# Performance work log

Hardware: AMD Instinct MI355X
Metric: run time of the kernel (lower is better)

Reference implementation:

```python
import jax, jax.numpy as jnp
import numpy as np

REG = 0.1          # entropic regularization, as in the module
N_ITERS = 100      # fixed Sinkhorn iteration count (POT numItermax capped; see notes)


def _sqdist(x, y):
    # ot.dist default: squared Euclidean pairwise distances, [n, m]
    x2 = jnp.sum(x * x, axis=1)[:, None]
    y2 = jnp.sum(y * y, axis=1)[None, :]
    M = x2 + y2 - 2.0 * (x @ y.T)
    return jnp.maximum(M, 0.0)


def setup_inputs() -> dict:
    key = jax.random.key(0)
    kx, ky = jax.random.split(key)
    n, m, d = 4096, 4096, 32
    # uniform in [0, 0.5) keeps exp(-M/reg) representable in fp32
    x = jax.random.uniform(kx, (n, d), dtype=jnp.float32) * 0.5
    y = jax.random.uniform(ky, (m, d), dtype=jnp.float32) * 0.5
    return {"x": x, "y": y}


def reference(x, y):
    n, m = x.shape[0], y.shape[0]
    a = jnp.full((n,), 1.0 / n, dtype=x.dtype)   # uniform source marginal
    b = jnp.full((m,), 1.0 / m, dtype=y.dtype)   # uniform target marginal
    M = _sqdist(x, y)                            # [n, m] cost
    K = jnp.exp(-M / REG)                        # [n, m] Gibbs kernel

    u0 = jnp.full((n,), 1.0 / n, dtype=x.dtype)
    v0 = jnp.full((m,), 1.0 / m, dtype=y.dtype)

    def step(carry, _):
        u, v = carry
        u = a / (K @ v)      # [n]
        v = b / (K.T @ u)    # [m]
        return (u, v), None

    (u, v), _ = jax.lax.scan(step, (u0, v0), None, length=N_ITERS)
    # transport plan gamma = diag(u) K diag(v), as returned by ot.bregman.sinkhorn
    gamma = u[:, None] * K * v[None, :]
    return gamma
```

## Files before the change

kernel.cpp:

```cpp
#include <hip/hip_runtime.h>
#include <hip/hip_fp16.h>


#define NN 4096
#define MM 4096
#define DD 32
#define N_ITERS 100

static constexpr float INV_REG = 10.0f;
static constexpr float A_MARG  = 1.0f / 4096.0f;
static constexpr float B_MARG  = 1.0f / 4096.0f;

typedef _Float16 h2_t __attribute__((ext_vector_type(2)));

static __device__ __forceinline__ float dot2(unsigned a, unsigned b, float acc) {
#if __has_builtin(__builtin_amdgcn_fdot2)
    return __builtin_amdgcn_fdot2(__builtin_bit_cast(h2_t, a),
                                  __builtin_bit_cast(h2_t, b), acc, false);
#else
    float2 fa = __half22float2(*(const __half2*)&a);
    float2 fb = __half22float2(*(const __half2*)&b);
    acc = fmaf(fa.x, fb.x, acc);
    return fmaf(fa.y, fb.y, acc);
#endif
}

static __device__ __forceinline__ unsigned ld_dev_u32(const unsigned* p) {
    return __hip_atomic_load(p, __ATOMIC_RELAXED, __HIP_MEMORY_SCOPE_AGENT);
}
static __device__ __forceinline__ void st_dev_u32(unsigned* p, unsigned v) {
    __hip_atomic_store(p, v, __ATOMIC_RELAXED, __HIP_MEMORY_SCOPE_AGENT);
}

__global__ void compute_K_half(const float* __restrict__ x, const float* __restrict__ y,
                               __half* __restrict__ Kh, __half* __restrict__ KTh,
                               unsigned* __restrict__ mbu, unsigned* __restrict__ mbv) {
    const int tid = threadIdx.x;
    const int j   = blockIdx.x * 256 + tid;
    const int r0  = blockIdx.y * 16;
    const int z   = blockIdx.z;
    const float* __restrict__ p = z ? y : x;
    const float* __restrict__ q = z ? x : y;
    __half* __restrict__ dst    = z ? KTh : Kh;

    if (z == 0 && blockIdx.y == 0) {
        mbu[j] = 0u;
        mbv[j] = 0u;
    }

    float qv[DD];
    const float4* q4 = (const float4*)(q + (size_t)j * DD);
#pragma unroll
    for (int k = 0; k < DD / 4; ++k) {
        float4 t = q4[k];
        qv[4 * k + 0] = t.x; qv[4 * k + 1] = t.y;
        qv[4 * k + 2] = t.z; qv[4 * k + 3] = t.w;
    }

    __shared__ float ps[16 * DD];
    ps[tid]       = p[(size_t)r0 * DD + tid];
    ps[tid + 256] = p[(size_t)r0 * DD + tid + 256];
    __syncthreads();

#pragma unroll 4
    for (int ii = 0; ii < 16; ++ii) {
        float acc = 0.0f;
#pragma unroll
        for (int k = 0; k < DD; ++k) {
            float d = ps[ii * DD + k] - qv[k];
            acc = fmaf(d, d, acc);
        }
        dst[(size_t)(r0 + ii) * MM + j] = __float2half(__expf(-acc * INV_REG));
    }
}

__global__ void __launch_bounds__(1024, 8)
sinkhorn_persist(const __half* __restrict__ Kh, const __half* __restrict__ KTh,
                 float* __restrict__ u32g, float* __restrict__ v32g,
                 unsigned* __restrict__ mbu, unsigned* __restrict__ mbv) {
    __shared__ __align__(16) __half vlds[MM];
    __shared__ float part[16];
    __shared__ unsigned fb_lds[8];
    const int tid  = threadIdx.x;
    const int lane = tid & 63;
    const int w    = tid >> 6;
    const int rib  = w >> 1;
    const int hlf  = w & 1;
    const int bid  = blockIdx.x;
    const int i    = bid * 8 + rib;
    const int g0   = hlf * 256 + lane;
    const uint4* __restrict__ MU = (const uint4*)(Kh  + (size_t)i * MM);
    const uint4* __restrict__ MV = (const uint4*)(KTh + (size_t)i * MM);
    unsigned short* __restrict__ vlh = (unsigned short*)vlds;

    const uint4 ku0 = MU[g0], ku1 = MU[g0 + 64], ku2 = MU[g0 + 128], ku3 = MU[g0 + 192];
    const uint4 kv0 = MV[g0], kv1 = MV[g0 + 64], kv2 = MV[g0 + 128], kv3 = MV[g0 + 192];

    unsigned histv = 0x10000u;

    for (int t = 0; t < N_ITERS; ++t) {
        if (t == 0) {
            if (tid < 512) {
                const unsigned long long dv =
                    (unsigned long long)__half_as_ushort(__float2half(B_MARG)) *
                    0x0001000100010001ULL;
                ((unsigned long long*)vlds)[2 * tid]     = dv;
                ((unsigned long long*)vlds)[2 * tid + 1] = dv;
            }
            __syncthreads();
        } else {
            if (tid < 512) {
                const unsigned want = (unsigned)(2 * t) & 0x7fffu;
                unsigned g[8];
#pragma unroll
                for (int k = 0; k < 8; ++k) g[k] = ld_dev_u32(mbv + (k << 9) + tid);
                for (;;) {
                    unsigned bad = 0u;
#pragma unroll
                    for (int k = 0; k < 8; ++k)
                        if ((g[k] & 0x7fffu) != want) bad |= 1u << k;
                    if (!bad) break;
                    __builtin_amdgcn_s_sleep(1);
#pragma unroll
                    for (int k = 0; k < 8; ++k)
                        if (bad & (1u << k)) g[k] = ld_dev_u32(mbv + (k << 9) + tid);
                }
                unsigned fzb = 0x8000u;
#pragma unroll
                for (int k = 0; k < 8; ++k) {
                    vlh[(k << 9) + tid] = (unsigned short)(g[k] >> 16);
                    fzb &= g[k];
                }
                const bool allf = __all(fzb != 0u);
                if ((tid & 63) == 0) fb_lds[tid >> 6] = allf ? 1u : 0u;
            }
            __syncthreads();
            if ((t & 1) == 0) {
                if ((fb_lds[0] & fb_lds[1] & fb_lds[2] & fb_lds[3] &
                     fb_lds[4] & fb_lds[5] & fb_lds[6] & fb_lds[7]) != 0u)
                    break;
            }
        }

        {
            const uint4* V = (const uint4*)vlds;
            const uint4 a = V[g0], b = V[g0 + 64], c = V[g0 + 128], d = V[g0 + 192];
            float x0 = 0.f, x1 = 0.f, x2 = 0.f, x3 = 0.f;
            x0 = dot2(ku0.x, a.x, x0); x0 = dot2(ku0.y, a.y, x0);
            x0 = dot2(ku0.z, a.z, x0); x0 = dot2(ku0.w, a.w, x0);
            x1 = dot2(ku1.x, b.x, x1); x1 = dot2(ku1.y, b.y, x1);
            x1 = dot2(ku1.z, b.z, x1); x1 = dot2(ku1.w, b.w, x1);
            x2 = dot2(ku2.x, c.x, x2); x2 = dot2(ku2.y, c.y, x2);
            x2 = dot2(ku2.z, c.z, x2); x2 = dot2(ku2.w, c.w, x2);
            x3 = dot2(ku3.x, d.x, x3); x3 = dot2(ku3.y, d.y, x3);
            x3 = dot2(ku3.z, d.z, x3); x3 = dot2(ku3.w, d.w, x3);
            float acc = (x0 + x1) + (x2 + x3);
#pragma unroll
            for (int off = 32; off > 0; off >>= 1) acc += __shfl_down(acc, off, 64);
            if (lane == 0) part[w] = acc;
        }
        __syncthreads();
        if (tid < 8) {
            float r = A_MARG / (part[2 * tid] + part[2 * tid + 1]);
            u32g[bid * 8 + tid] = r;
            const unsigned val = (unsigned)__half_as_ushort(__float2half(r));
            st_dev_u32(mbu + bid * 8 + tid,
                       (val << 16) | ((unsigned)(2 * t + 1) & 0x7fffu));
        }

        if (tid < 512) {
            const unsigned want = (unsigned)(2 * t + 1) & 0x7fffu;
            unsigned g[8];
#pragma unroll
            for (int k = 0; k < 8; ++k) g[k] = ld_dev_u32(mbu + (k << 9) + tid);
            for (;;) {
                unsigned bad = 0u;
#pragma unroll
                for (int k = 0; k < 8; ++k)
                    if ((g[k] & 0x7fffu) != want) bad |= 1u << k;
                if (!bad) break;
                __builtin_amdgcn_s_sleep(1);
#pragma unroll
                for (int k = 0; k < 8; ++k)
                    if (bad & (1u << k)) g[k] = ld_dev_u32(mbu + (k << 9) + tid);
            }
#pragma unroll
            for (int k = 0; k < 8; ++k)
                vlh[(k << 9) + tid] = (unsigned short)(g[k] >> 16);
        }
        __syncthreads();

        {
            const uint4* V = (const uint4*)vlds;
            const uint4 a = V[g0], b = V[g0 + 64], c = V[g0 + 128], d = V[g0 + 192];
            float x0 = 0.f, x1 = 0.f, x2 = 0.f, x3 = 0.f;
            x0 = dot2(kv0.x, a.x, x0); x0 = dot2(kv0.y, a.y, x0);
            x0 = dot2(kv0.z, a.z, x0); x0 = dot2(kv0.w, a.w, x0);
            x1 = dot2(kv1.x, b.x, x1); x1 = dot2(kv1.y, b.y, x1);
            x1 = dot2(kv1.z, b.z, x1); x1 = dot2(kv1.w, b.w, x1);
            x2 = dot2(kv2.x, c.x, x2); x2 = dot2(kv2.y, c.y, x2);
            x2 = dot2(kv2.z, c.z, x2); x2 = dot2(kv2.w, c.w, x2);
            x3 = dot2(kv3.x, d.x, x3); x3 = dot2(kv3.y, d.y, x3);
            x3 = dot2(kv3.z, d.z, x3); x3 = dot2(kv3.w, d.w, x3);
            float acc = (x0 + x1) + (x2 + x3);
#pragma unroll
            for (int off = 32; off > 0; off >>= 1) acc += __shfl_down(acc, off, 64);
            if (lane == 0) part[w] = acc;
        }
        __syncthreads();
        if (tid < 8) {
            float r = B_MARG / (part[2 * tid] + part[2 * tid + 1]);
            v32g[bid * 8 + tid] = r;
            const unsigned val = (unsigned)__half_as_ushort(__float2half(r));
            unsigned ph = (unsigned)(2 * t + 2) & 0x7fffu;
            if (t & 1) {
                if (val == histv) ph |= 0x8000u;
                histv = val;
            }
            st_dev_u32(mbv + bid * 8 + tid, (val << 16) | ph);
        }
    }
}

__global__ void epilogue(const float* __restrict__ x, const float* __restrict__ y,
                         const float* __restrict__ u, const float* __restrict__ v,
                         float* __restrict__ out) {
    const int tid = threadIdx.x;
    const int j   = blockIdx.x * 256 + tid;
    const int r0  = blockIdx.y * 16;

    float yv[DD];
    const float4* y4 = (const float4*)(y + (size_t)j * DD);
#pragma unroll
    for (int k = 0; k < DD / 4; ++k) {
        float4 t = y4[k];
        yv[4 * k + 0] = t.x; yv[4 * k + 1] = t.y;
        yv[4 * k + 2] = t.z; yv[4 * k + 3] = t.w;
    }

    __shared__ float xs[16 * DD];
    __shared__ float u_lds[16];
    xs[tid]       = x[(size_t)r0 * DD + tid];
    xs[tid + 256] = x[(size_t)r0 * DD + tid + 256];
    if (tid < 16) u_lds[tid] = u[r0 + tid];
    __syncthreads();

    const float vj = v[j];
#pragma unroll 4
    for (int ii = 0; ii < 16; ++ii) {
        float acc = 0.0f;
#pragma unroll
        for (int k = 0; k < DD; ++k) {
            float d = xs[ii * DD + k] - yv[k];
            acc = fmaf(d, d, acc);
        }
        out[(size_t)(r0 + ii) * MM + j] = u_lds[ii] * __expf(-acc * INV_REG) * vj;
    }
}

extern "C" void kernel_launch(void* const* d_in, const int* in_sizes, int n_in,
                              void* d_out, int out_size, void* d_ws, size_t ws_size,
                              hipStream_t stream) {
    const float* x = (const float*)d_in[0];
    const float* y = (const float*)d_in[1];
    __half*   Kh   = (__half*)d_ws;
    __half*   KTh  = Kh + (size_t)NN * MM;
    float*    u32  = (float*)(KTh + (size_t)NN * MM);
    float*    v32  = u32 + NN;
    unsigned* mbu  = (unsigned*)(v32 + MM);
    unsigned* mbv  = mbu + NN;
    float*    out  = (float*)d_out;

    compute_K_half<<<dim3(16, 256, 2), 256, 0, stream>>>(x, y, Kh, KTh, mbu, mbv);

    sinkhorn_persist<<<512, 1024, 0, stream>>>(Kh, KTh, u32, v32, mbu, mbv);

    epilogue<<<dim3(MM / 256, NN / 16), 256, 0, stream>>>(x, y, u32, v32, out);
}
```

Measured before the change: 539.4 us.

## Assign one full row per wave and halve persistent grid to 256 blocks

Each wave now owns an entire K and K^T row (8 uint4 chunks per lane held in registers), so the cross-wave partial-sum LDS exchange and its extra __syncthreads are removed. Lane 0 of each wave writes its result directly to the mailbox. Separate LDS buffers for the u and v vectors drop one barrier per half-iteration. The grid shrinks to 256 blocks of 16 rows each, which halves the number of global mailbox pollers, at the cost of higher register pressure (launch bounds lowered to 4) and longer per-wave dot-product chains.

```diff
diff --git a/kernel.cpp b/kernel.cpp
--- a/kernel.cpp
+++ b/kernel.cpp
@@ -74,150 +74,171 @@
     }
 }
 
-__global__ void __launch_bounds__(1024, 8)
+__global__ void __launch_bounds__(1024, 4)
 sinkhorn_persist(const __half* __restrict__ Kh, const __half* __restrict__ KTh,
                  float* __restrict__ u32g, float* __restrict__ v32g,
                  unsigned* __restrict__ mbu, unsigned* __restrict__ mbv) {
-    __shared__ __align__(16) __half vlds[MM];
-    __shared__ float part[16];
-    __shared__ unsigned fb_lds[8];
+    __shared__ __align__(16) __half vbuf0[MM];
+    __shared__ __align__(16) __half vbuf1[MM];
+    __shared__ unsigned fb_lds[16];
     const int tid  = threadIdx.x;
     const int lane = tid & 63;
     const int w    = tid >> 6;
-    const int rib  = w >> 1;
-    const int hlf  = w & 1;
     const int bid  = blockIdx.x;
-    const int i    = bid * 8 + rib;
-    const int g0   = hlf * 256 + lane;
+    const int i    = bid * 16 + w;
     const uint4* __restrict__ MU = (const uint4*)(Kh  + (size_t)i * MM);
     const uint4* __restrict__ MV = (const uint4*)(KTh + (size_t)i * MM);
-    unsigned short* __restrict__ vlh = (unsigned short*)vlds;
-
-    const uint4 ku0 = MU[g0], ku1 = MU[g0 + 64], ku2 = MU[g0 + 128], ku3 = MU[g0 + 192];
-    const uint4 kv0 = MV[g0], kv1 = MV[g0 + 64], kv2 = MV[g0 + 128], kv3 = MV[g0 + 192];
+    unsigned short* __restrict__ vl0 = (unsigned short*)vbuf0;
+    unsigned short* __restrict__ vl1 = (unsigned short*)vbuf1;
+
+    uint4 ku[8], kv[8];
+#pragma unroll
+    for (int c = 0; c < 8; ++c) ku[c] = MU[lane + 64 * c];
+#pragma unroll
+    for (int c = 0; c < 8; ++c) kv[c] = MV[lane + 64 * c];
 
     unsigned histv = 0x10000u;
 
+    {
+        const unsigned long long dv =
+            (unsigned long long)__half_as_ushort(__float2half(B_MARG)) *
+            0x0001000100010001ULL;
+        ((unsigned long long*)vbuf0)[tid] = dv;
+    }
+
     for (int t = 0; t < N_ITERS; ++t) {
-        if (t == 0) {
-            if (tid < 512) {
-                const unsigned long long dv =
-                    (unsigned long long)__half_as_ushort(__float2half(B_MARG)) *
-                    0x0001000100010001ULL;
-                ((unsigned long long*)vlds)[2 * tid]     = dv;
-                ((unsigned long long*)vlds)[2 * tid + 1] = dv;
-            }
-            __syncthreads();
-        } else {
-            if (tid < 512) {
-                const unsigned want = (unsigned)(2 * t) & 0x7fffu;
-                unsigned g[8];
-#pragma unroll
-                for (int k = 0; k < 8; ++k) g[k] = ld_dev_u32(mbv + (k << 9) + tid);
-                for (;;) {
-                    unsigned bad = 0u;
-#pragma unroll
-                    for (int k = 0; k < 8; ++k)
-                        if ((g[k] & 0x7fffu) != want) bad |= 1u << k;
-                    if (!bad) break;
-                    __builtin_amdgcn_s_sleep(1);
-#pragma unroll
-                    for (int k = 0; k < 8; ++k)
-                        if (bad & (1u << k)) g[k] = ld_dev_u32(mbv + (k << 9) + tid);
-                }
-                unsigned fzb = 0x8000u;
-#pragma unroll
-                for (int k = 0; k < 8; ++k) {
-                    vlh[(k << 9) + tid] = (unsigned short)(g[k] >> 16);
-                    fzb &= g[k];
-                }
-                const bool allf = __all(fzb != 0u);
-                if ((tid & 63) == 0) fb_lds[tid >> 6] = allf ? 1u : 0u;
-            }
-            __syncthreads();
-            if ((t & 1) == 0) {
-                if ((fb_lds[0] & fb_lds[1] & fb_lds[2] & fb_lds[3] &
-                     fb_lds[4] & fb_lds[5] & fb_lds[6] & fb_lds[7]) != 0u)
-                    break;
-            }
-        }
-
-        {
-            const uint4* V = (const uint4*)vlds;
-            const uint4 a = V[g0], b = V[g0 + 64], c = V[g0 + 128], d = V[g0 + 192];
-            float x0 = 0.f, x1 = 0.f, x2 = 0.f, x3 = 0.f;
-            x0 = dot2(ku0.x, a.x, x0); x0 = dot2(ku0.y, a.y, x0);
-            x0 = dot2(ku0.z, a.z, x0); x0 = dot2(ku0.w, a.w, x0);
-            x1 = dot2(ku1.x, b.x, x1); x1 = dot2(ku1.y, b.y, x1);
-            x1 = dot2(ku1.z, b.z, x1); x1 = dot2(ku1.w, b.w, x1);
-            x2 = dot2(ku2.x, c.x, x2); x2 = dot2(ku2.y, c.y, x2);
-            x2 = dot2(ku2.z, c.z, x2); x2 = dot2(ku2.w, c.w, x2);
-            x3 = dot2(ku3.x, d.x, x3); x3 = dot2(ku3.y, d.y, x3);
-            x3 = dot2(ku3.z, d.z, x3); x3 = dot2(ku3.w, d.w, x3);
-            float acc = (x0 + x1) + (x2 + x3);
-#pragma unroll
-            for (int off = 32; off > 0; off >>= 1) acc += __shfl_down(acc, off, 64);
-            if (lane == 0) part[w] = acc;
-        }
-        __syncthreads();
-        if (tid < 8) {
-            float r = A_MARG / (part[2 * tid] + part[2 * tid + 1]);
-            u32g[bid * 8 + tid] = r;
-            const unsigned val = (unsigned)__half_as_ushort(__float2half(r));
-            st_dev_u32(mbu + bid * 8 + tid,
-                       (val << 16) | ((unsigned)(2 * t + 1) & 0x7fffu));
-        }
-
-        if (tid < 512) {
-            const unsigned want = (unsigned)(2 * t + 1) & 0x7fffu;
-            unsigned g[8];
-#pragma unroll
-            for (int k = 0; k < 8; ++k) g[k] = ld_dev_u32(mbu + (k << 9) + tid);
+        if (t != 0) {
+            const unsigned want = (unsigned)(2 * t) & 0x7fffu;
+            unsigned g[4];
+#pragma unroll
+            for (int k = 0; k < 4; ++k) g[k] = ld_dev_u32(mbv + (k << 10) + tid);
             for (;;) {
                 unsigned bad = 0u;
 #pragma unroll
-                for (int k = 0; k < 8; ++k)
+                for (int k = 0; k < 4; ++k)
                     if ((g[k] & 0x7fffu) != want) bad |= 1u << k;
                 if (!bad) break;
                 __builtin_amdgcn_s_sleep(1);
 #pragma unroll
-                for (int k = 0; k < 8; ++k)
-                    if (bad & (1u << k)) g[k] = ld_dev_u32(mbu + (k << 9) + tid);
-            }
-#pragma unroll
-            for (int k = 0; k < 8; ++k)
-                vlh[(k << 9) + tid] = (unsigned short)(g[k] >> 16);
+                for (int k = 0; k < 4; ++k)
+                    if (bad & (1u << k)) g[k] = ld_dev_u32(mbv + (k << 10) + tid);
+            }
+            unsigned fzb = 0x8000u;
+#pragma unroll
+            for (int k = 0; k < 4; ++k) {
+                vl0[(k << 10) + tid] = (unsigned short)(g[k] >> 16);
+                fzb &= g[k];
+            }
+            const bool allf = __all(fzb != 0u);
+            if (lane == 0) fb_lds[w] = allf ? 1u : 0u;
         }
         __syncthreads();
+        if (t != 0 && (t & 1) == 0) {
+            unsigned f = 1u;
+#pragma unroll
+            for (int q = 0; q < 16; ++q) f &= fb_lds[q];
+            if (f) break;
+        }
 
         {
-            const uint4* V = (const uint4*)vlds;
-            const uint4 a = V[g0], b = V[g0 + 64], c = V[g0 + 128], d = V[g0 + 192];
+            const uint4* V = (const uint4*)vbuf0;
+            uint4 a0 = V[lane], a1 = V[lane + 64], a2 = V[lane + 128], a3 = V[lane + 192];
+            uint4 a4 = V[lane + 256], a5 = V[lane + 320], a6 = V[lane + 384], a7 = V[lane + 448];
             float x0 = 0.f, x1 = 0.f, x2 = 0.f, x3 = 0.f;
-            x0 = dot2(kv0.x, a.x, x0); x0 = dot2(kv0.y, a.y, x0);
-            x0 = dot2(kv0.z, a.z, x0); x0 = dot2(kv0.w, a.w, x0);
-            x1 = dot2(kv1.x, b.x, x1); x1 = dot2(kv1.y, b.y, x1);
-            x1 = dot2(kv1.z, b.z, x1); x1 = dot2(kv1.w, b.w, x1);
-            x2 = dot2(kv2.x, c.x, x2); x2 = dot2(kv2.y, c.y, x2);
-            x2 = dot2(kv2.z, c.z, x2); x2 = dot2(kv2.w, c.w, x2);
-            x3 = dot2(kv3.x, d.x, x3); x3 = dot2(kv3.y, d.y, x3);
-            x3 = dot2(kv3.z, d.z, x3); x3 = dot2(kv3.w, d.w, x3);
-            float acc = (x0 + x1) + (x2 + x3);
-#pragma unroll
-            for (int off = 32; off > 0; off >>= 1) acc += __shfl_down(acc, off, 64);
-            if (lane == 0) part[w] = acc;
+            float x4 = 0.f, x5 = 0.f, x6 = 0.f, x7 = 0.f;
+            x0 = dot2(ku[0].x, a0.x, x0); x0 = dot2(ku[0].y, a0.y, x0);
+            x0 = dot2(ku[0].z, a0.z, x0); x0 = dot2(ku[0].w, a0.w, x0);
+            x1 = dot2(ku[1].x, a1.x, x1); x1 = dot2(ku[1].y, a1.y, x1);
+            x1 = dot2(ku[1].z, a1.z, x1); x1 = dot2(ku[1].w, a1.w, x1);
+            x2 = dot2(ku[2].x, a2.x, x2); x2 = dot2(ku[2].y, a2.y, x2);
+            x2 = dot2(ku[2].z, a2.z, x2); x2 = dot2(ku[2].w, a2.w, x2);
+            x3 = dot2(ku[3].x, a3.x, x3); x3 = dot2(ku[3].y, a3.y, x3);
+            x3 = dot2(ku[3].z, a3.z, x3); x3 = dot2(ku[3].w, a3.w, x3);
+            x4 = dot2(ku[4].x, a4.x, x4); x4 = dot2(ku[4].y, a4.y, x4);
+            x4 = dot2(ku[4].z, a4.z, x4); x4 = dot2(ku[4].w, a4.w, x4);
+            x5 = dot2(ku[5].x, a5.x, x5); x5 = dot2(ku[5].y, a5.y, x5);
+            x5 = dot2(ku[5].z, a5.z, x5); x5 = dot2(ku[5].w, a5.w, x5);
+            x6 = dot2(ku[6].x, a6.x, x6); x6 = dot2(ku[6].y, a6.y, x6);
+            x6 = dot2(ku[6].z, a6.z, x6); x6 = dot2(ku[6].w, a6.w, x6);
+            x7 = dot2(ku[7].x, a7.x, x7); x7 = dot2(ku[7].y, a7.y, x7);
+            x7 = dot2(ku[7].z, a7.z, x7); x7 = dot2(ku[7].w, a7.w, x7);
+            float s0 = (x0 + x1) + (x2 + x3);
+            float s1 = (x4 + x5) + (x6 + x7);
+#pragma unroll
+            for (int off = 32; off > 0; off >>= 1) {
+                s0 += __shfl_down(s0, off, 64);
+                s1 += __shfl_down(s1, off, 64);
+            }
+            if (lane == 0) {
+                float r = A_MARG / (s0 + s1);
+                u32g[i] = r;
+                const unsigned val = (unsigned)__half_as_ushort(__float2half(r));
+                st_dev_u32(mbu + i, (val << 16) | ((unsigned)(2 * t + 1) & 0x7fffu));
+            }
+        }
+
+        {
+            const unsigned want = (unsigned)(2 * t + 1) & 0x7fffu;
+            unsigned g[4];
+#pragma unroll
+            for (int k = 0; k < 4; ++k) g[k] = ld_dev_u32(mbu + (k << 10) + tid);
+            for (;;) {
+                unsigned bad = 0u;
+#pragma unroll
+                for (int k = 0; k < 4; ++k)
+                    if ((g[k] & 0x7fffu) != want) bad |= 1u << k;
+                if (!bad) break;
+                __builtin_amdgcn_s_sleep(1);
+#pragma unroll
+                for (int k = 0; k < 4; ++k)
+                    if (bad & (1u << k)) g[k] = ld_dev_u32(mbu + (k << 10) + tid);
+            }
+#pragma unroll
+            for (int k = 0; k < 4; ++k)
+                vl1[(k << 10) + tid] = (unsigned short)(g[k] >> 16);
         }
         __syncthreads();
-        if (tid < 8) {
-            float r = B_MARG / (part[2 * tid] + part[2 * tid + 1]);
-            v32g[bid * 8 + tid] = r;
-            const unsigned val = (unsigned)__half_as_ushort(__float2half(r));
-            unsigned ph = (unsigned)(2 * t + 2) & 0x7fffu;
-            if (t & 1) {
-                if (val == histv) ph |= 0x8000u;
-                histv = val;
-            }
-            st_dev_u32(mbv + bid * 8 + tid, (val << 16) | ph);
+
+        {
+            const uint4* V = (const uint4*)vbuf1;
+            uint4 a0 = V[lane], a1 = V[lane + 64], a2 = V[lane + 128], a3 = V[lane + 192];
+            uint4 a4 = V[lane + 256], a5 = V[lane + 320], a6 = V[lane + 384], a7 = V[lane + 448];
+            float x0 = 0.f, x1 = 0.f, x2 = 0.f, x3 = 0.f;
+            float x4 = 0.f, x5 = 0.f, x6 = 0.f, x7 = 0.f;
+            x0 = dot2(kv[0].x, a0.x, x0); x0 = dot2(kv[0].y, a0.y, x0);
+            x0 = dot2(kv[0].z, a0.z, x0); x0 = dot2(kv[0].w, a0.w, x0);
+            x1 = dot2(kv[1].x, a1.x, x1); x1 = dot2(kv[1].y, a1.y, x1);
+            x1 = dot2(kv[1].z, a1.z, x1); x1 = dot2(kv[1].w, a1.w, x1);
+            x2 = dot2(kv[2].x, a2.x, x2); x2 = dot2(kv[2].y, a2.y, x2);
+            x2 = dot2(kv[2].z, a2.z, x2); x2 = dot2(kv[2].w, a2.w, x2);
+            x3 = dot2(kv[3].x, a3.x, x3); x3 = dot2(kv[3].y, a3.y, x3);
+            x3 = dot2(kv[3].z, a3.z, x3); x3 = dot2(kv[3].w, a3.w, x3);
+            x4 = dot2(kv[4].x, a4.x, x4); x4 = dot2(kv[4].y, a4.y, x4);
+            x4 = dot2(kv[4].z, a4.z, x4); x4 = dot2(kv[4].w, a4.w, x4);
+            x5 = dot2(kv[5].x, a5.x, x5); x5 = dot2(kv[5].y, a5.y, x5);
+            x5 = dot2(kv[5].z, a5.z, x5); x5 = dot2(kv[5].w, a5.w, x5);
+            x6 = dot2(kv[6].x, a6.x, x6); x6 = dot2(kv[6].y, a6.y, x6);
+            x6 = dot2(kv[6].z, a6.z, x6); x6 = dot2(kv[6].w, a6.w, x6);
+            x7 = dot2(kv[7].x, a7.x, x7); x7 = dot2(kv[7].y, a7.y, x7);
+            x7 = dot2(kv[7].z, a7.z, x7); x7 = dot2(kv[7].w, a7.w, x7);
+            float s0 = (x0 + x1) + (x2 + x3);
+            float s1 = (x4 + x5) + (x6 + x7);
+#pragma unroll
+            for (int off = 32; off > 0; off >>= 1) {
+                s0 += __shfl_down(s0, off, 64);
+                s1 += __shfl_down(s1, off, 64);
+            }
+            if (lane == 0) {
+                float r = B_MARG / (s0 + s1);
+                v32g[i] = r;
+                const unsigned val = (unsigned)__half_as_ushort(__float2half(r));
+                unsigned ph = (unsigned)(2 * t + 2) & 0x7fffu;
+                if (t & 1) {
+                    if (val == histv) ph |= 0x8000u;
+                    histv = val;
+                }
+                st_dev_u32(mbv + i, (val << 16) | ph);
+            }
         }
     }
 }
@@ -273,7 +294,7 @@
 
     compute_K_half<<<dim3(16, 256, 2), 256, 0, stream>>>(x, y, Kh, KTh, mbu, mbv);
 
-    sinkhorn_persist<<<512, 1024, 0, stream>>>(Kh, KTh, u32, v32, mbu, mbv);
+    sinkhorn_persist<<<256, 1024, 0, stream>>>(Kh, KTh, u32, v32, mbu, mbv);
 
     epilogue<<<dim3(MM / 256, NN / 16), 256, 0, stream>>>(x, y, u32, v32, out);
 }
```

Result: slower. 554.0 us (+2.7%).

## Fuse epilogue into persistent Sinkhorn kernel and widen mailbox polling to 64-bit

Applied to the files above, without the earlier changes.

Folds the transport-plan epilogue into the persistent Sinkhorn kernel. Each block publishes its final fp32 v through a new flag-initialised mailbox and keeps u in registers, which removes a kernel launch and the global u/v round trip. Mailbox polling now uses all 1024 threads with 64-bit relaxed loads instead of 512 threads doing eight 32-bit loads each, which shortens the per-iteration barrier exchange. The trade-off is that the epilogue now runs on only 512 blocks with a wider per-thread loop, which may lower its parallelism.

```diff
diff --git a/kernel.cpp b/kernel.cpp
--- a/kernel.cpp
+++ b/kernel.cpp
@@ -31,10 +31,14 @@
 static __device__ __forceinline__ void st_dev_u32(unsigned* p, unsigned v) {
     __hip_atomic_store(p, v, __ATOMIC_RELAXED, __HIP_MEMORY_SCOPE_AGENT);
 }
+static __device__ __forceinline__ unsigned long long ld_dev_u64(const unsigned long long* p) {
+    return __hip_atomic_load(p, __ATOMIC_RELAXED, __HIP_MEMORY_SCOPE_AGENT);
+}
 
 __global__ void compute_K_half(const float* __restrict__ x, const float* __restrict__ y,
                                __half* __restrict__ Kh, __half* __restrict__ KTh,
-                               unsigned* __restrict__ mbu, unsigned* __restrict__ mbv) {
+                               unsigned* __restrict__ mbu, unsigned* __restrict__ mbv,
+                               unsigned* __restrict__ mbv32) {
     const int tid = threadIdx.x;
     const int j   = blockIdx.x * 256 + tid;
     const int r0  = blockIdx.y * 16;
@@ -44,8 +48,9 @@
     __half* __restrict__ dst    = z ? KTh : Kh;
 
     if (z == 0 && blockIdx.y == 0) {
-        mbu[j] = 0u;
-        mbv[j] = 0u;
+        mbu[j]   = 0u;
+        mbv[j]   = 0u;
+        mbv32[j] = 0xFFFFFFFFu;
     }
 
     float qv[DD];
@@ -75,12 +80,17 @@
 }
 
 __global__ void __launch_bounds__(1024, 8)
-sinkhorn_persist(const __half* __restrict__ Kh, const __half* __restrict__ KTh,
-                 float* __restrict__ u32g, float* __restrict__ v32g,
-                 unsigned* __restrict__ mbu, unsigned* __restrict__ mbv) {
+sinkhorn_all(const float* __restrict__ x, const float* __restrict__ y,
+             const __half* __restrict__ Kh, const __half* __restrict__ KTh,
+             float* __restrict__ out,
+             unsigned* __restrict__ mbu, unsigned* __restrict__ mbv,
+             unsigned* __restrict__ mbv32) {
     __shared__ __align__(16) __half vlds[MM];
+    __shared__ float vfin[MM];
+    __shared__ float xs[8 * DD];
+    __shared__ float ufin[8];
     __shared__ float part[16];
-    __shared__ unsigned fb_lds[8];
+    __shared__ unsigned fb_lds[16];
     const int tid  = threadIdx.x;
     const int lane = tid & 63;
     const int w    = tid >> 6;
@@ -91,55 +101,51 @@
     const int g0   = hlf * 256 + lane;
     const uint4* __restrict__ MU = (const uint4*)(Kh  + (size_t)i * MM);
     const uint4* __restrict__ MV = (const uint4*)(KTh + (size_t)i * MM);
-    unsigned short* __restrict__ vlh = (unsigned short*)vlds;
+    const unsigned long long* __restrict__ mbv64 = (const unsigned long long*)mbv;
+    const unsigned long long* __restrict__ mbu64 = (const unsigned long long*)mbu;
 
     const uint4 ku0 = MU[g0], ku1 = MU[g0 + 64], ku2 = MU[g0 + 128], ku3 = MU[g0 + 192];
     const uint4 kv0 = MV[g0], kv1 = MV[g0 + 64], kv2 = MV[g0 + 128], kv3 = MV[g0 + 192];
 
     unsigned histv = 0x10000u;
+    float u_last = 0.0f, v_last = 0.0f;
+
+    const unsigned long long PHMASK = 0x00007FFF00007FFFull;
+    const unsigned long long FZMASK = 0x0000800000008000ull;
 
     for (int t = 0; t < N_ITERS; ++t) {
         if (t == 0) {
-            if (tid < 512) {
-                const unsigned long long dv =
-                    (unsigned long long)__half_as_ushort(__float2half(B_MARG)) *
-                    0x0001000100010001ULL;
-                ((unsigned long long*)vlds)[2 * tid]     = dv;
-                ((unsigned long long*)vlds)[2 * tid + 1] = dv;
-            }
-            __syncthreads();
+            const unsigned long long dv =
+                (unsigned long long)__half_as_ushort(__float2half(B_MARG)) *
+                0x0001000100010001ULL;
+            ((unsigned long long*)vlds)[tid] = dv;
         } else {
-            if (tid < 512) {
-                const unsigned want = (unsigned)(2 * t) & 0x7fffu;
-                unsigned g[8];
-#pragma unroll
-                for (int k = 0; k < 8; ++k) g[k] = ld_dev_u32(mbv + (k << 9) + tid);
-                for (;;) {
-                    unsigned bad = 0u;
-#pragma unroll
-                    for (int k = 0; k < 8; ++k)
-                        if ((g[k] & 0x7fffu) != want) bad |= 1u << k;
-                    if (!bad) break;
-                    __builtin_amdgcn_s_sleep(1);
-#pragma unroll
-                    for (int k = 0; k < 8; ++k)
-                        if (bad & (1u << k)) g[k] = ld_dev_u32(mbv + (k << 9) + tid);
-                }
-                unsigned fzb = 0x8000u;
-#pragma unroll
-                for (int k = 0; k < 8; ++k) {
-                    vlh[(k << 9) + tid] = (unsigned short)(g[k] >> 16);
-                    fzb &= g[k];
-                }
-                const bool allf = __all(fzb != 0u);
-                if ((tid & 63) == 0) fb_lds[tid >> 6] = allf ? 1u : 0u;
-            }
-            __syncthreads();
-            if ((t & 1) == 0) {
-                if ((fb_lds[0] & fb_lds[1] & fb_lds[2] & fb_lds[3] &
-                     fb_lds[4] & fb_lds[5] & fb_lds[6] & fb_lds[7]) != 0u)
-                    break;
-            }
+            const unsigned long long wantp =
+                ((unsigned long long)((2 * t) & 0x7fff)) * 0x0000000100000001ull;
+            unsigned long long g0v = ld_dev_u64(mbv64 + tid);
+            unsigned long long g1v = ld_dev_u64(mbv64 + tid + 1024);
+            while ((g0v & PHMASK) != wantp) {
+                __builtin_amdgcn_s_sleep(1);
+                g0v = ld_dev_u64(mbv64 + tid);
+            }
+            while ((g1v & PHMASK) != wantp) {
+                __builtin_amdgcn_s_sleep(1);
+                g1v = ld_dev_u64(mbv64 + tid + 1024);
+            }
+            ((unsigned*)vlds)[tid] =
+                (unsigned)(((g0v >> 16) & 0xFFFFull) | (((g0v >> 48) & 0xFFFFull) << 16));
+            ((unsigned*)vlds)[tid + 1024] =
+                (unsigned)(((g1v >> 16) & 0xFFFFull) | (((g1v >> 48) & 0xFFFFull) << 16));
+            const bool allf = __all(((g0v & FZMASK) == FZMASK) &&
+                                    ((g1v & FZMASK) == FZMASK));
+            if (lane == 0) fb_lds[w] = allf ? 1u : 0u;
+        }
+        __syncthreads();
+        if (t != 0 && (t & 1) == 0) {
+            unsigned f = 1u;
+#pragma unroll
+            for (int q = 0; q < 16; ++q) f &= fb_lds[q];
+            if (f) break;
         }
 
         {
@@ -162,31 +168,29 @@
         __syncthreads();
         if (tid < 8) {
             float r = A_MARG / (part[2 * tid] + part[2 * tid + 1]);
-            u32g[bid * 8 + tid] = r;
+            u_last = r;
             const unsigned val = (unsigned)__half_as_ushort(__float2half(r));
             st_dev_u32(mbu + bid * 8 + tid,
                        (val << 16) | ((unsigned)(2 * t + 1) & 0x7fffu));
         }
 
-        if (tid < 512) {
-            const unsigned want = (unsigned)(2 * t + 1) & 0x7fffu;
-            unsigned g[8];
-#pragma unroll
-            for (int k = 0; k < 8; ++k) g[k] = ld_dev_u32(mbu + (k << 9) + tid);
-            for (;;) {
-                unsigned bad = 0u;
-#pragma unroll
-                for (int k = 0; k < 8; ++k)
-                    if ((g[k] & 0x7fffu) != want) bad |= 1u << k;
-                if (!bad) break;
-                __builtin_amdgcn_s_sleep(1);
-#pragma unroll
-                for (int k = 0; k < 8; ++k)
-                    if (bad & (1u << k)) g[k] = ld_dev_u32(mbu + (k << 9) + tid);
-            }
-#pragma unroll
-            for (int k = 0; k < 8; ++k)
-                vlh[(k << 9) + tid] = (unsigned short)(g[k] >> 16);
+        {
+            const unsigned long long wantp =
+                ((unsigned long long)((2 * t + 1) & 0x7fff)) * 0x0000000100000001ull;
+            unsigned long long g0v = ld_dev_u64(mbu64 + tid);
+            unsigned long long g1v = ld_dev_u64(mbu64 + tid + 1024);
+            while ((g0v & PHMASK) != wantp) {
+                __builtin_amdgcn_s_sleep(1);
+                g0v = ld_dev_u64(mbu64 + tid);
+            }
+            while ((g1v & PHMASK) != wantp) {
+                __builtin_amdgcn_s_sleep(1);
+                g1v = ld_dev_u64(mbu64 + tid + 1024);
+            }
+            ((unsigned*)vlds)[tid] =
+                (unsigned)(((g0v >> 16) & 0xFFFFull) | (((g0v >> 48) & 0xFFFFull) << 16));
+            ((unsigned*)vlds)[tid + 1024] =
+                (unsigned)(((g1v >> 16) & 0xFFFFull) | (((g1v >> 48) & 0xFFFFull) << 16));
         }
         __syncthreads();
 
@@ -210,7 +214,7 @@
         __syncthreads();
         if (tid < 8) {
             float r = B_MARG / (part[2 * tid] + part[2 * tid + 1]);
-            v32g[bid * 8 + tid] = r;
+            v_last = r;
             const unsigned val = (unsigned)__half_as_ushort(__float2half(r));
             unsigned ph = (unsigned)(2 * t + 2) & 0x7fffu;
             if (t & 1) {
@@ -220,41 +224,47 @@
             st_dev_u32(mbv + bid * 8 + tid, (val << 16) | ph);
         }
     }
-}
-
-__global__ void epilogue(const float* __restrict__ x, const float* __restrict__ y,
-                         const float* __restrict__ u, const float* __restrict__ v,
-                         float* __restrict__ out) {
-    const int tid = threadIdx.x;
-    const int j   = blockIdx.x * 256 + tid;
-    const int r0  = blockIdx.y * 16;
-
-    float yv[DD];
-    const float4* y4 = (const float4*)(y + (size_t)j * DD);
-#pragma unroll
-    for (int k = 0; k < DD / 4; ++k) {
-        float4 t = y4[k];
-        yv[4 * k + 0] = t.x; yv[4 * k + 1] = t.y;
-        yv[4 * k + 2] = t.z; yv[4 * k + 3] = t.w;
-    }
-
-    __shared__ float xs[16 * DD];
-    __shared__ float u_lds[16];
-    xs[tid]       = x[(size_t)r0 * DD + tid];
-    xs[tid + 256] = x[(size_t)r0 * DD + tid + 256];
-    if (tid < 16) u_lds[tid] = u[r0 + tid];
+
+    if (tid < 8) {
+        st_dev_u32(mbv32 + bid * 8 + tid, __float_as_uint(v_last));
+        ufin[tid] = u_last;
+    }
+    if (tid < 8 * DD) xs[tid] = x[(size_t)(bid * 8) * DD + tid];
+
+#pragma unroll
+    for (int k = 0; k < 4; ++k) {
+        const int idx = (k << 10) + tid;
+        unsigned wv = ld_dev_u32(mbv32 + idx);
+        while (wv >> 31) {
+            __builtin_amdgcn_s_sleep(1);
+            wv = ld_dev_u32(mbv32 + idx);
+        }
+        vfin[idx] = __uint_as_float(wv);
+    }
     __syncthreads();
 
-    const float vj = v[j];
-#pragma unroll 4
-    for (int ii = 0; ii < 16; ++ii) {
-        float acc = 0.0f;
-#pragma unroll
-        for (int k = 0; k < DD; ++k) {
-            float d = xs[ii * DD + k] - yv[k];
-            acc = fmaf(d, d, acc);
-        }
-        out[(size_t)(r0 + ii) * MM + j] = u_lds[ii] * __expf(-acc * INV_REG) * vj;
+#pragma unroll
+    for (int k = 0; k < 4; ++k) {
+        const int j = (k << 10) + tid;
+        float yv[DD];
+        const float4* y4 = (const float4*)(y + (size_t)j * DD);
+#pragma unroll
+        for (int q = 0; q < DD / 4; ++q) {
+            float4 tq = y4[q];
+            yv[4 * q + 0] = tq.x; yv[4 * q + 1] = tq.y;
+            yv[4 * q + 2] = tq.z; yv[4 * q + 3] = tq.w;
+        }
+        const float vj = vfin[j];
+#pragma unroll
+        for (int r = 0; r < 8; ++r) {
+            float acc = 0.0f;
+#pragma unroll
+            for (int q = 0; q < DD; ++q) {
+                float d = xs[r * DD + q] - yv[q];
+                acc = fmaf(d, d, acc);
+            }
+            out[(size_t)(bid * 8 + r) * MM + j] = ufin[r] * __expf(-acc * INV_REG) * vj;
+        }
     }
 }
 
@@ -263,17 +273,14 @@
                               hipStream_t stream) {
     const float* x = (const float*)d_in[0];
     const float* y = (const float*)d_in[1];
-    __half*   Kh   = (__half*)d_ws;
-    __half*   KTh  = Kh + (size_t)NN * MM;
-    float*    u32  = (float*)(KTh + (size_t)NN * MM);
-    float*    v32  = u32 + NN;
-    unsigned* mbu  = (unsigned*)(v32 + MM);
-    unsigned* mbv  = mbu + NN;
-    float*    out  = (float*)d_out;
-
-    compute_K_half<<<dim3(16, 256, 2), 256, 0, stream>>>(x, y, Kh, KTh, mbu, mbv);
-
-    sinkhorn_persist<<<512, 1024, 0, stream>>>(Kh, KTh, u32, v32, mbu, mbv);
-
-    epilogue<<<dim3(MM / 256, NN / 16), 256, 0, stream>>>(x, y, u32, v32, out);
-}
+    __half*   Kh    = (__half*)d_ws;
+    __half*   KTh   = Kh + (size_t)NN * MM;
+    unsigned* mbu   = (unsigned*)(KTh + (size_t)NN * MM);
+    unsigned* mbv   = mbu + NN;
+    unsigned* mbv32 = mbv + NN;
+    float*    out   = (float*)d_out;
+
+    compute_K_half<<<dim3(16, 256, 2), 256, 0, stream>>>(x, y, Kh, KTh, mbu, mbv, mbv32);
+
+    sinkhorn_all<<<512, 1024, 0, stream>>>(x, y, Kh, KTh, out, mbu, mbv, mbv32);
+}
```

Result: slower. 1.171 ms (+117.1%).
